# Optimization experiments

Measured on AMD Instinct MI355X. Metric: run time of the kernel, lower is better.

## Reference

```python
import jax, jax.numpy as jnp
import numpy as np

BIG_NEG = -1.0e6  # constants.big_negative


def setup_inputs() -> dict:
    key = jax.random.key(0)
    ks = jax.random.split(key, 10)
    B, N, NF, HNF, M, T = 2048, 100, 128, 128, 128, 12
    hidden_output_nodes = jax.random.normal(ks[0], (B, N, HNF), dtype=jnp.float32)
    input_nodes = jax.random.normal(ks[1], (B, N, NF), dtype=jnp.float32)
    node_mask = jax.random.uniform(ks[2], (B, N)) < 0.8
    node_mask = node_mask.at[:, 0].set(True)  # avoid fully-masked rows
    s = 0.05
    W_emb = jax.random.normal(ks[3], (M, NF + HNF), dtype=jnp.float32) * s
    b_emb = jnp.zeros((M,), dtype=jnp.float32)
    W_ih = jax.random.normal(ks[4], (4 * M, M), dtype=jnp.float32) * s
    b_ih = jnp.zeros((4 * M,), dtype=jnp.float32)
    W_hh = jax.random.normal(ks[5], (4 * M, M), dtype=jnp.float32) * s
    b_hh = jnp.zeros((4 * M,), dtype=jnp.float32)
    return {
        "hidden_output_nodes": hidden_output_nodes,
        "input_nodes": input_nodes,
        "W_emb": W_emb, "b_emb": b_emb,
        "W_ih": W_ih, "b_ih": b_ih, "W_hh": W_hh, "b_hh": b_hh,
        "node_mask": node_mask,
        "lstm_computations": T,
    }


def _set2vec(hidden_output_nodes, input_nodes, W_emb, b_emb, W_ih, b_ih, W_hh, b_hh, node_mask, T):
    B = input_nodes.shape[0]
    M = W_emb.shape[0]
    # memory: [B, N, M]
    cat = jnp.concatenate((hidden_output_nodes, input_nodes), axis=2)
    memory = jnp.einsum("bnf,mf->bnm", cat, W_emb) + b_emb
    energy_mask = (~node_mask).astype(memory.dtype) * BIG_NEG  # [B, N]

    zeros = jnp.zeros((B, M), dtype=memory.dtype)

    def step(carry, _):
        lstm_in, h, c = carry
        # LSTMCell (PyTorch gate order: i, f, g, o)
        gates = lstm_in @ W_ih.T + b_ih + h @ W_hh.T + b_hh
        i, f, g, o = jnp.split(gates, 4, axis=-1)
        c = jax.nn.sigmoid(f) * c + jax.nn.sigmoid(i) * jnp.tanh(g)
        q = jax.nn.sigmoid(o) * jnp.tanh(c)  # query / new hidden state
        # dot-product attention read over the node memory
        energies = jnp.einsum("bm,bnm->bn", q, memory) + energy_mask
        attn = jax.nn.softmax(energies, axis=1)
        read = jnp.einsum("bn,bnm->bm", attn, memory)
        return (read, q, c), None

    (read, q, _), _ = jax.lax.scan(step, (zeros, zeros, zeros), None, length=T)
    return jnp.concatenate((q, read), axis=1)  # [B, 2*M]


def reference(hidden_output_nodes, input_nodes, W_emb, b_emb, W_ih, b_ih, W_hh, b_hh, node_mask, lstm_computations):
    return _set2vec(hidden_output_nodes, input_nodes, W_emb, b_emb, W_ih, b_ih, W_hh, b_hh, node_mask, lstm_computations)
```

## Files before the change

### kernel.cpp

```cpp
#include <hip/hip_runtime.h>
#include <hip/hip_fp16.h>
#include <math.h>

#define BIG_NEG  (-1.0e6f)
#define NN   100
#define MD   128
#define KD   256
#define G4   512
#define NB   4
#define MP2  68
#define XPAD 288

#define WS_WGF_H  32768
#define WS_BIAS_F 81920

typedef _Float16 f16x2 __attribute__((ext_vector_type(2)));
typedef _Float16 f16x8 __attribute__((ext_vector_type(8)));
typedef float    f32x4 __attribute__((ext_vector_type(4)));

#if __has_builtin(__builtin_amdgcn_rcpf)
#define RCPF(x) __builtin_amdgcn_rcpf(x)
#else
#define RCPF(x) (1.0f / (x))
#endif

#define PKRTZ(a, b) __builtin_bit_cast(unsigned, __builtin_amdgcn_cvt_pkrtz((a), (b)))

__device__ __forceinline__ float sigm(float x) {
    return RCPF(1.0f + __expf(-x));
}
__device__ __forceinline__ float tanh_f(float x) {
    float xc = fminf(fmaxf(x, -15.0f), 15.0f);
    float e  = __expf(2.0f * xc);
    return (e - 1.0f) * RCPF(e + 1.0f);
}

extern "C" __global__ void prep_kernel(const float* __restrict__ W_emb,
                                       const float* __restrict__ W_ih,
                                       const float* __restrict__ b_ih,
                                       const float* __restrict__ W_hh,
                                       const float* __restrict__ b_hh,
                                       float* __restrict__ ws) {
    int tid = blockIdx.x * blockDim.x + threadIdx.x;
    int nth = gridDim.x * blockDim.x;
    __half* WF    = (__half*)ws;
    __half* WG    = (__half*)ws + WS_WGF_H;
    float*  biasc = ws + WS_BIAS_F;
    for (int i = tid; i < 32768; i += nth) {
        int kg = i >> 10, m = (i >> 3) & 127, j = i & 7;
        WF[i] = __float2half(W_emb[m * 256 + kg * 8 + j]);
    }
    for (int i = tid; i < 131072; i += nth) {
        int kc = i >> 12, g = (i >> 3) & 511, j = i & 7;
        int k = kc * 8 + j;
        float w = (k < 128) ? W_ih[g * 128 + k] : W_hh[g * 128 + (k - 128)];
        WG[i] = __float2half(w);
    }
    for (int i = tid; i < 512; i += nth) biasc[i] = b_ih[i] + b_hh[i];
}

extern "C" __global__ __launch_bounds__(1024, 4)
void set2vec_main(const float* __restrict__ hidden,
                  const float* __restrict__ input,
                  const float* __restrict__ b_emb,
                  const unsigned char* __restrict__ mask_bytes,
                  const int* __restrict__ Tptr,
                  const float* __restrict__ ws,
                  float* __restrict__ out) {
    __shared__ __half2 mem2[NB][NN][MP2];
    __shared__ __half  xcath[NB][XPAD];
    __shared__ float   xcat2[NB][KD];
    __shared__ float   cbuf[NB][MD];
    __shared__ float   emask[NB][NN];
    __shared__ float   bbuf[G4];
    __shared__ int     mask_is_u8;
    __shared__ float   gbuf[NB][G4];
    __shared__ float   ebuf[NB][128];
    __shared__ float   abuf[NB][NN];

    const int tid  = threadIdx.x;
    const int b0   = blockIdx.x * NB;
    const int lane = tid & 63, wv = tid >> 6;
    const int ln15 = lane & 15, lhi = lane >> 4;
    const __half* WF   = (const __half*)ws;
    const __half* memh = (const __half*)mem2;

    if (tid == 0) {
        int nz = 0;
        for (int i = 0; i < 64; ++i)
            if ((i & 3) && mask_bytes[i]) nz = 1;
        mask_is_u8 = nz;
    }

    {
        const float be0 = b_emb[0 * 16 + ln15], be1 = b_emb[1 * 16 + ln15];
        const float be2 = b_emb[2 * 16 + ln15], be3 = b_emb[3 * 16 + ln15];
        const float be4 = b_emb[4 * 16 + ln15], be5 = b_emb[5 * 16 + ln15];
        const float be6 = b_emb[6 * 16 + ln15], be7 = b_emb[7 * 16 + ln15];
        __half* memw = (__half*)mem2;
        for (int tile = wv; tile < 25; tile += 16) {
            f32x4 acc0 = {be0, be0, be0, be0}, acc1 = {be1, be1, be1, be1};
            f32x4 acc2 = {be2, be2, be2, be2}, acc3 = {be3, be3, be3, be3};
            f32x4 acc4 = {be4, be4, be4, be4}, acc5 = {be5, be5, be5, be5};
            f32x4 acc6 = {be6, be6, be6, be6}, acc7 = {be7, be7, be7, be7};

            const int rA     = tile * 16 + ln15;
            const int rAok   = rA < NB * NN;
            const long gbase = ((long)(b0 * NN + rA)) << 7;

            #pragma unroll 1
            for (int mk = 0; mk < 8; ++mk) {
                f16x8 aF;
                if (rAok) {
                    int k0 = mk * 32 + lhi * 8;
                    const float* src = (k0 < 128) ? (hidden + gbase + k0)
                                                  : (input + gbase + (k0 - 128));
                    float4 v0 = *(const float4*)src;
                    float4 v1 = *(const float4*)(src + 4);
                    union { f16x8 v; unsigned u[4]; } au;
                    au.u[0] = PKRTZ(v0.x, v0.y);
                    au.u[1] = PKRTZ(v0.z, v0.w);
                    au.u[2] = PKRTZ(v1.x, v1.y);
                    au.u[3] = PKRTZ(v1.z, v1.w);
                    aF = au.v;
                } else {
                    aF = (f16x8)(_Float16)0.0f;
                }
                const __half* wrow = WF + ((mk * 4 + lhi) * 128 + ln15) * 8;
#define EMB_CT(CT, ACC) { \
                union { uint4 u; f16x8 v; } bu; \
                bu.u = *(const uint4*)(wrow + (CT * 16) * 8); \
                ACC = __builtin_amdgcn_mfma_f32_16x16x32_f16(aF, bu.v, ACC, 0, 0, 0); }
                EMB_CT(0, acc0) EMB_CT(1, acc1) EMB_CT(2, acc2) EMB_CT(3, acc3)
                EMB_CT(4, acc4) EMB_CT(5, acc5) EMB_CT(6, acc6) EMB_CT(7, acc7)
#undef EMB_CT
            }
#define EMB_WR(CT, ACC) { \
            _Pragma("unroll") \
            for (int reg = 0; reg < 4; ++reg) { \
                int r = tile * 16 + lhi * 4 + reg; \
                if (r < NB * NN) { \
                    int bb = r / NN, n = r - (r / NN) * NN; \
                    memw[(bb * NN + n) * (2 * MP2) + CT * 16 + ln15] = __float2half(ACC[reg]); \
                } } }
            EMB_WR(0, acc0) EMB_WR(1, acc1) EMB_WR(2, acc2) EMB_WR(3, acc3)
            EMB_WR(4, acc4) EMB_WR(5, acc5) EMB_WR(6, acc6) EMB_WR(7, acc7)
#undef EMB_WR
        }
    }

    const uint4* WgB = (const uint4*)((const __half*)ws + WS_WGF_H);
    const int ct0 = wv * 2, ct1 = wv * 2 + 1;
#define LDW(KS) \
    const uint4 wA##KS = WgB[((KS) * 4 + lhi) * 512 + ct0 * 16 + ln15]; \
    const uint4 wB##KS = WgB[((KS) * 4 + lhi) * 512 + ct1 * 16 + ln15];
    LDW(0) LDW(1) LDW(2) LDW(3) LDW(4) LDW(5) LDW(6) LDW(7)
#undef LDW

    for (int i = tid; i < NB * XPAD; i += 1024) ((__half*)xcath)[i] = __float2half(0.0f);
    ((float*)xcat2)[tid] = 0.0f;
    if (tid < NB * MD) ((float*)cbuf)[tid] = 0.0f;
    if (tid < G4) bbuf[tid] = ws[WS_BIAS_F + tid];
    if (tid < NB * NN) {
        int bb = tid / NN, n = tid - bb * NN;
        long mrow = (long)(b0 + bb) * NN + n;
        int valid = mask_is_u8 ? (mask_bytes[mrow] != 0)
                               : (((const int*)mask_bytes)[mrow] != 0);
        emask[bb][n] = valid ? 0.0f : BIG_NEG;
    }
    __syncthreads();

    const int T = Tptr[0];

    const __half* aBase = &xcath[ln15 & 3][lhi * 8];

    const int ep0 = wv * 2, ep1 = wv * 2 + 1;
    const int e_bb0 = ep0 / 7, e_nt0 = ep0 - e_bb0 * 7;
    const int e_bb1 = ep1 / 7, e_nt1 = ep1 - e_bb1 * 7;
    const int e_n0  = e_nt0 * 16 + ln15, e_n1 = e_nt1 * 16 + ln15;
    const int e_n0c = (e_n0 < 100) ? e_n0 : 99;
    const int e_n1c = (e_n1 < 100) ? e_n1 : 99;
    const __half* eB0 = memh + (e_bb0 * NN + e_n0c) * (2 * MP2) + lhi * 8;
    const __half* eB1 = memh + (e_bb1 * NN + e_n1c) * (2 * MP2) + lhi * 8;
    const __half* eA0 = &xcath[e_bb0][128 + lhi * 8];
    const __half* eA1 = &xcath[e_bb1][128 + lhi * 8];

    const int sr_bb = (wv >> 1) & 3, sr_mh = wv & 1;
    const int rg = lane >> 3, rs = lane & 7;
    const int r_start = (rg <= 4) ? rg * 13 : 64 + (rg - 5) * 12;
    const int r_cnt   = (rg < 4) ? 13 : 12;
    const __half* rB = memh + sr_bb * NN * (2 * MP2) + sr_mh * 64 + rs * 8;

    for (int step = 0; step < T; ++step) {
        {
            f32x4 ga = {0.f, 0.f, 0.f, 0.f}, gb = {0.f, 0.f, 0.f, 0.f};
#define GS(KS) { \
            union { uint4 u; f16x8 v; } a, ba, bc; \
            a.u  = *(const uint4*)(aBase + (KS) * 32); \
            ba.u = wA##KS; bc.u = wB##KS; \
            ga = __builtin_amdgcn_mfma_f32_16x16x32_f16(a.v, ba.v, ga, 0, 0, 0); \
            gb = __builtin_amdgcn_mfma_f32_16x16x32_f16(a.v, bc.v, gb, 0, 0, 0); }
            GS(0) GS(1) GS(2) GS(3) GS(4) GS(5) GS(6) GS(7)
#undef GS
            if (lhi == 0) {
                #pragma unroll
                for (int r = 0; r < 4; ++r) {
                    gbuf[r][ct0 * 16 + ln15] = ga[r];
                    gbuf[r][ct1 * 16 + ln15] = gb[r];
                }
            }
        }
        __syncthreads();
        if (tid < NB * MD) {
            int bb = tid >> 7, m = tid & 127;
            float gi = gbuf[bb][m]       + bbuf[m];
            float gf = gbuf[bb][128 + m] + bbuf[128 + m];
            float gg = gbuf[bb][256 + m] + bbuf[256 + m];
            float go = gbuf[bb][384 + m] + bbuf[384 + m];
            float c  = cbuf[bb][m];
            c = sigm(gf) * c + sigm(gi) * tanh_f(gg);
            float qv = sigm(go) * tanh_f(c);
            cbuf[bb][m] = c;
            xcat2[bb][128 + m] = qv;
            xcath[bb][128 + m] = __float2half(qv);
        }
        __syncthreads();
        if (wv < 14) {
            f32x4 e0 = {0.f, 0.f, 0.f, 0.f}, e1 = {0.f, 0.f, 0.f, 0.f};
#define ES(KS) { \
            union { uint4 u; f16x8 v; } a0, a1, bq0, bq1; \
            a0.u  = *(const uint4*)(eA0 + (KS) * 32); \
            bq0.u = *(const uint4*)(eB0 + (KS) * 32); \
            a1.u  = *(const uint4*)(eA1 + (KS) * 32); \
            bq1.u = *(const uint4*)(eB1 + (KS) * 32); \
            e0 = __builtin_amdgcn_mfma_f32_16x16x32_f16(a0.v, bq0.v, e0, 0, 0, 0); \
            e1 = __builtin_amdgcn_mfma_f32_16x16x32_f16(a1.v, bq1.v, e1, 0, 0, 0); }
            ES(0) ES(1) ES(2) ES(3)
#undef ES
            if (lhi == 0) {
                if (e_n0 < 100) ebuf[e_bb0][e_n0] = e0[0] + emask[e_bb0][e_n0];
                if (e_n1 < 100) ebuf[e_bb1][e_n1] = e1[0] + emask[e_bb1][e_n1];
            }
        }
        __syncthreads();
        if (wv < 8) {
            {
                float e0 = ebuf[sr_bb][lane];
                float e1 = (lane < 36) ? ebuf[sr_bb][64 + lane] : -INFINITY;
                float mx = fmaxf(e0, e1);
                for (int off = 32; off; off >>= 1) mx = fmaxf(mx, __shfl_xor(mx, off, 64));
                float p0 = __expf(e0 - mx);
                float p1 = (lane < 36) ? __expf(e1 - mx) : 0.0f;
                float s = p0 + p1;
                for (int off = 32; off; off >>= 1) s += __shfl_xor(s, off, 64);
                float inv = RCPF(s);
                abuf[sr_bb][lane] = p0 * inv;
                if (lane < 36) abuf[sr_bb][64 + lane] = p1 * inv;
            }
            float a0 = 0.f, a1 = 0.f, a2 = 0.f, a3 = 0.f;
            float a4 = 0.f, a5 = 0.f, a6 = 0.f, a7 = 0.f;
            #pragma unroll
            for (int j = 0; j < 13; ++j) {
                if (j < r_cnt) {
                    int n = r_start + j;
                    float av = abuf[sr_bb][n];
                    uint4 u  = *(const uint4*)(rB + n * (2 * MP2));
                    float2 f0 = __half22float2(*(__half2*)&u.x);
                    float2 f1 = __half22float2(*(__half2*)&u.y);
                    float2 f2 = __half22float2(*(__half2*)&u.z);
                    float2 f3 = __half22float2(*(__half2*)&u.w);
                    a0 = fmaf(av, f0.x, a0); a1 = fmaf(av, f0.y, a1);
                    a2 = fmaf(av, f1.x, a2); a3 = fmaf(av, f1.y, a3);
                    a4 = fmaf(av, f2.x, a4); a5 = fmaf(av, f2.y, a5);
                    a6 = fmaf(av, f3.x, a6); a7 = fmaf(av, f3.y, a7);
                }
            }
#define RED(A) A += __shfl_xor(A, 8, 64); A += __shfl_xor(A, 16, 64); A += __shfl_xor(A, 32, 64);
            RED(a0) RED(a1) RED(a2) RED(a3) RED(a4) RED(a5) RED(a6) RED(a7)
#undef RED
            if (lane < 8) {
                int m = sr_mh * 64 + lane * 8;
                float4 lo = {a0, a1, a2, a3}, hi = {a4, a5, a6, a7};
                *(float4*)&xcat2[sr_bb][m]     = lo;
                *(float4*)&xcat2[sr_bb][m + 4] = hi;
                uint4 hv;
                hv.x = PKRTZ(a0, a1);
                hv.y = PKRTZ(a2, a3);
                hv.z = PKRTZ(a4, a5);
                hv.w = PKRTZ(a6, a7);
                *(uint4*)&xcath[sr_bb][m] = hv;
            }
        }
        __syncthreads();
    }

    {
        int bb = tid >> 8, j = tid & 255;
        float v = (j < 128) ? xcat2[bb][128 + j] : xcat2[bb][j - 128];
        out[((long)(b0 + bb) << 8) + j] = v;
    }
}

extern "C" void kernel_launch(void* const* d_in, const int* in_sizes, int n_in,
                              void* d_out, int out_size, void* d_ws, size_t ws_size,
                              hipStream_t stream) {
    const float* hidden = (const float*)d_in[0];
    const float* input  = (const float*)d_in[1];
    const float* W_emb  = (const float*)d_in[2];
    const float* b_emb  = (const float*)d_in[3];
    const float* W_ih   = (const float*)d_in[4];
    const float* b_ih   = (const float*)d_in[5];
    const float* W_hh   = (const float*)d_in[6];
    const float* b_hh   = (const float*)d_in[7];
    const unsigned char* mask = (const unsigned char*)d_in[8];
    const int*  Tptr    = (const int*)d_in[9];
    float* ws   = (float*)d_ws;
    float* outp = (float*)d_out;

    hipLaunchKernelGGL(prep_kernel, dim3(128), dim3(256), 0, stream,
                       W_emb, W_ih, b_ih, W_hh, b_hh, ws);
    hipLaunchKernelGGL(set2vec_main, dim3(512), dim3(1024), 0, stream,
                       hidden, input, b_emb, mask, Tptr, ws, outp);
}
```

Before: 165.5 us.

## Halve batch rows per block and reload LSTM weights each step

Cuts the batch elements per workgroup from 4 to 2 and doubles the grid to 1024 blocks. The embedding, energy and attention-read work is redistributed across waves to match. The per-wave register-resident gate weights are dropped, and weights are now reloaded from global memory (likely L2) at every LSTM step, freeing registers. The aim is more blocks in flight and lower per-block latency on the serial recurrence, at the cost of repeated weight traffic and MFMA tiles that are only half-used on rows.

```diff
diff --git a/kernel.cpp b/kernel.cpp
--- a/kernel.cpp
+++ b/kernel.cpp
@@ -7,7 +7,7 @@
 #define MD   128
 #define KD   256
 #define G4   512
-#define NB   4
+#define NB   2
 #define MP2  68
 #define XPAD 288
 
@@ -98,7 +98,8 @@
         const float be4 = b_emb[4 * 16 + ln15], be5 = b_emb[5 * 16 + ln15];
         const float be6 = b_emb[6 * 16 + ln15], be7 = b_emb[7 * 16 + ln15];
         __half* memw = (__half*)mem2;
-        for (int tile = wv; tile < 25; tile += 16) {
+        const int tile = wv;
+        if (tile < 13) {
             f32x4 acc0 = {be0, be0, be0, be0}, acc1 = {be1, be1, be1, be1};
             f32x4 acc2 = {be2, be2, be2, be2}, acc3 = {be3, be3, be3, be3};
             f32x4 acc4 = {be4, be4, be4, be4}, acc5 = {be5, be5, be5, be5};
@@ -151,14 +152,9 @@
 
     const uint4* WgB = (const uint4*)((const __half*)ws + WS_WGF_H);
     const int ct0 = wv * 2, ct1 = wv * 2 + 1;
-#define LDW(KS) \
-    const uint4 wA##KS = WgB[((KS) * 4 + lhi) * 512 + ct0 * 16 + ln15]; \
-    const uint4 wB##KS = WgB[((KS) * 4 + lhi) * 512 + ct1 * 16 + ln15];
-    LDW(0) LDW(1) LDW(2) LDW(3) LDW(4) LDW(5) LDW(6) LDW(7)
-#undef LDW
 
     for (int i = tid; i < NB * XPAD; i += 1024) ((__half*)xcath)[i] = __float2half(0.0f);
-    ((float*)xcat2)[tid] = 0.0f;
+    if (tid < NB * KD) ((float*)xcat2)[tid] = 0.0f;
     if (tid < NB * MD) ((float*)cbuf)[tid] = 0.0f;
     if (tid < G4) bbuf[tid] = ws[WS_BIAS_F + tid];
     if (tid < NB * NN) {
@@ -172,24 +168,20 @@
 
     const int T = Tptr[0];
 
-    const __half* aBase = &xcath[ln15 & 3][lhi * 8];
-
-    const int ep0 = wv * 2, ep1 = wv * 2 + 1;
-    const int e_bb0 = ep0 / 7, e_nt0 = ep0 - e_bb0 * 7;
-    const int e_bb1 = ep1 / 7, e_nt1 = ep1 - e_bb1 * 7;
-    const int e_n0  = e_nt0 * 16 + ln15, e_n1 = e_nt1 * 16 + ln15;
-    const int e_n0c = (e_n0 < 100) ? e_n0 : 99;
-    const int e_n1c = (e_n1 < 100) ? e_n1 : 99;
-    const __half* eB0 = memh + (e_bb0 * NN + e_n0c) * (2 * MP2) + lhi * 8;
-    const __half* eB1 = memh + (e_bb1 * NN + e_n1c) * (2 * MP2) + lhi * 8;
-    const __half* eA0 = &xcath[e_bb0][128 + lhi * 8];
-    const __half* eA1 = &xcath[e_bb1][128 + lhi * 8];
-
-    const int sr_bb = (wv >> 1) & 3, sr_mh = wv & 1;
-    const int rg = lane >> 3, rs = lane & 7;
-    const int r_start = (rg <= 4) ? rg * 13 : 64 + (rg - 5) * 12;
-    const int r_cnt   = (rg < 4) ? 13 : 12;
-    const __half* rB = memh + sr_bb * NN * (2 * MP2) + sr_mh * 64 + rs * 8;
+    const __half* aBase = &xcath[ln15 & 1][lhi * 8];
+
+    const int e_bb = (wv < 14) ? (wv / 7) : 0;
+    const int e_nt = (wv < 14) ? (wv - e_bb * 7) : 0;
+    const int e_n  = e_nt * 16 + ln15;
+    const int e_nc = (e_n < 100) ? e_n : 99;
+    const __half* eB = memh + (e_bb * NN + e_nc) * (2 * MP2) + lhi * 8;
+    const __half* eA = &xcath[e_bb][128 + lhi * 8];
+
+    const int sr_bb = (wv >> 2) & 1, sr_mq = wv & 3;
+    const int rg = lane >> 2, rs = lane & 3;
+    const int r_start = (rg < 4) ? rg * 7 : 28 + (rg - 4) * 6;
+    const int r_cnt   = (rg < 4) ? 7 : 6;
+    const __half* rB = memh + sr_bb * NN * (2 * MP2) + sr_mq * 32 + rs * 8;
 
     for (int step = 0; step < T; ++step) {
         {
@@ -197,17 +189,17 @@
 #define GS(KS) { \
             union { uint4 u; f16x8 v; } a, ba, bc; \
             a.u  = *(const uint4*)(aBase + (KS) * 32); \
-            ba.u = wA##KS; bc.u = wB##KS; \
+            ba.u = WgB[((KS) * 4 + lhi) * 512 + ct0 * 16 + ln15]; \
+            bc.u = WgB[((KS) * 4 + lhi) * 512 + ct1 * 16 + ln15]; \
             ga = __builtin_amdgcn_mfma_f32_16x16x32_f16(a.v, ba.v, ga, 0, 0, 0); \
             gb = __builtin_amdgcn_mfma_f32_16x16x32_f16(a.v, bc.v, gb, 0, 0, 0); }
             GS(0) GS(1) GS(2) GS(3) GS(4) GS(5) GS(6) GS(7)
 #undef GS
             if (lhi == 0) {
-                #pragma unroll
-                for (int r = 0; r < 4; ++r) {
-                    gbuf[r][ct0 * 16 + ln15] = ga[r];
-                    gbuf[r][ct1 * 16 + ln15] = gb[r];
-                }
+                gbuf[0][ct0 * 16 + ln15] = ga[0];
+                gbuf[1][ct0 * 16 + ln15] = ga[1];
+                gbuf[0][ct1 * 16 + ln15] = gb[0];
+                gbuf[1][ct1 * 16 + ln15] = gb[1];
             }
         }
         __syncthreads();
@@ -226,21 +218,16 @@
         }
         __syncthreads();
         if (wv < 14) {
-            f32x4 e0 = {0.f, 0.f, 0.f, 0.f}, e1 = {0.f, 0.f, 0.f, 0.f};
+            f32x4 e0 = {0.f, 0.f, 0.f, 0.f};
 #define ES(KS) { \
-            union { uint4 u; f16x8 v; } a0, a1, bq0, bq1; \
-            a0.u  = *(const uint4*)(eA0 + (KS) * 32); \
-            bq0.u = *(const uint4*)(eB0 + (KS) * 32); \
-            a1.u  = *(const uint4*)(eA1 + (KS) * 32); \
-            bq1.u = *(const uint4*)(eB1 + (KS) * 32); \
-            e0 = __builtin_amdgcn_mfma_f32_16x16x32_f16(a0.v, bq0.v, e0, 0, 0, 0); \
-            e1 = __builtin_amdgcn_mfma_f32_16x16x32_f16(a1.v, bq1.v, e1, 0, 0, 0); }
+            union { uint4 u; f16x8 v; } a0, bq0; \
+            a0.u  = *(const uint4*)(eA + (KS) * 32); \
+            bq0.u = *(const uint4*)(eB + (KS) * 32); \
+            e0 = __builtin_amdgcn_mfma_f32_16x16x32_f16(a0.v, bq0.v, e0, 0, 0, 0); }
             ES(0) ES(1) ES(2) ES(3)
 #undef ES
-            if (lhi == 0) {
-                if (e_n0 < 100) ebuf[e_bb0][e_n0] = e0[0] + emask[e_bb0][e_n0];
-                if (e_n1 < 100) ebuf[e_bb1][e_n1] = e1[0] + emask[e_bb1][e_n1];
-            }
+            if (lhi == 0 && e_n < 100)
+                ebuf[e_bb][e_n] = e0[0] + emask[e_bb][e_n];
         }
         __syncthreads();
         if (wv < 8) {
@@ -260,7 +247,7 @@
             float a0 = 0.f, a1 = 0.f, a2 = 0.f, a3 = 0.f;
             float a4 = 0.f, a5 = 0.f, a6 = 0.f, a7 = 0.f;
             #pragma unroll
-            for (int j = 0; j < 13; ++j) {
+            for (int j = 0; j < 7; ++j) {
                 if (j < r_cnt) {
                     int n = r_start + j;
                     float av = abuf[sr_bb][n];
@@ -275,11 +262,12 @@
                     a6 = fmaf(av, f3.x, a6); a7 = fmaf(av, f3.y, a7);
                 }
             }
-#define RED(A) A += __shfl_xor(A, 8, 64); A += __shfl_xor(A, 16, 64); A += __shfl_xor(A, 32, 64);
+#define RED(A) A += __shfl_xor(A, 4, 64); A += __shfl_xor(A, 8, 64); \
+               A += __shfl_xor(A, 16, 64); A += __shfl_xor(A, 32, 64);
             RED(a0) RED(a1) RED(a2) RED(a3) RED(a4) RED(a5) RED(a6) RED(a7)
 #undef RED
-            if (lane < 8) {
-                int m = sr_mh * 64 + lane * 8;
+            if (lane < 4) {
+                int m = sr_mq * 32 + lane * 8;
                 float4 lo = {a0, a1, a2, a3}, hi = {a4, a5, a6, a7};
                 *(float4*)&xcat2[sr_bb][m]     = lo;
                 *(float4*)&xcat2[sr_bb][m + 4] = hi;
@@ -294,7 +282,7 @@
         __syncthreads();
     }
 
-    {
+    if (tid < NB * 256) {
         int bb = tid >> 8, j = tid & 255;
         float v = (j < 128) ? xcat2[bb][128 + j] : xcat2[bb][j - 128];
         out[((long)(b0 + bb) << 8) + j] = v;
@@ -319,6 +307,6 @@
 
     hipLaunchKernelGGL(prep_kernel, dim3(128), dim3(256), 0, stream,
                        W_emb, W_ih, b_ih, W_hh, b_hh, ws);
-    hipLaunchKernelGGL(set2vec_main, dim3(512), dim3(1024), 0, stream,
+    hipLaunchKernelGGL(set2vec_main, dim3(1024), dim3(1024), 0, stream,
                        hidden, input, b_emb, mask, Tptr, ws, outp);
 }
```

Result: slower. 236.5 us (+42.9%).

## Fuse LSTM pointwise into gate MFMA via interleaved gates and double-buffered inputs

Applied to the files above, without the earlier changes.

Gate weight rows and biases are permuted so each 4-lane group holds the i,f,g,o gates for one hidden unit. The LSTM cell update then runs in registers via cross-lane shuffles right after the gate MFMA, which removes the gbuf round trip and one barrier per step. The LSTM input vector is double-buffered so the next step's q and read can be written without a race, and the attention read now spreads over all 16 waves with finer row splits. In exchange, the gate weights are reloaded from global memory every step instead of staying in registers, which adds memory latency in the recurrent loop.

```diff
diff --git a/kernel.cpp b/kernel.cpp
--- a/kernel.cpp
+++ b/kernel.cpp
@@ -51,12 +51,16 @@
         WF[i] = __float2half(W_emb[m * 256 + kg * 8 + j]);
     }
     for (int i = tid; i < 131072; i += nth) {
-        int kc = i >> 12, g = (i >> 3) & 511, j = i & 7;
+        int kc = i >> 12, gp = (i >> 3) & 511, j = i & 7;
         int k = kc * 8 + j;
+        int g = (gp & 3) * 128 + (gp >> 2);
         float w = (k < 128) ? W_ih[g * 128 + k] : W_hh[g * 128 + (k - 128)];
         WG[i] = __float2half(w);
     }
-    for (int i = tid; i < 512; i += nth) biasc[i] = b_ih[i] + b_hh[i];
+    for (int i = tid; i < 512; i += nth) {
+        int g = (i & 3) * 128 + (i >> 2);
+        biasc[i] = b_ih[g] + b_hh[g];
+    }
 }
 
 extern "C" __global__ __launch_bounds__(1024, 4)
@@ -68,13 +72,12 @@
                   const float* __restrict__ ws,
                   float* __restrict__ out) {
     __shared__ __half2 mem2[NB][NN][MP2];
-    __shared__ __half  xcath[NB][XPAD];
+    __shared__ __half  xh[2][NB][XPAD];
     __shared__ float   xcat2[NB][KD];
     __shared__ float   cbuf[NB][MD];
     __shared__ float   emask[NB][NN];
     __shared__ float   bbuf[G4];
     __shared__ int     mask_is_u8;
-    __shared__ float   gbuf[NB][G4];
     __shared__ float   ebuf[NB][128];
     __shared__ float   abuf[NB][NN];
 
@@ -151,13 +154,9 @@
 
     const uint4* WgB = (const uint4*)((const __half*)ws + WS_WGF_H);
     const int ct0 = wv * 2, ct1 = wv * 2 + 1;
-#define LDW(KS) \
-    const uint4 wA##KS = WgB[((KS) * 4 + lhi) * 512 + ct0 * 16 + ln15]; \
-    const uint4 wB##KS = WgB[((KS) * 4 + lhi) * 512 + ct1 * 16 + ln15];
-    LDW(0) LDW(1) LDW(2) LDW(3) LDW(4) LDW(5) LDW(6) LDW(7)
-#undef LDW
-
-    for (int i = tid; i < NB * XPAD; i += 1024) ((__half*)xcath)[i] = __float2half(0.0f);
+    const int gp0 = ct0 * 16 + ln15, gp1 = ct1 * 16 + ln15;
+
+    for (int i = tid; i < 2 * NB * XPAD; i += 1024) ((__half*)xh)[i] = __float2half(0.0f);
     ((float*)xcat2)[tid] = 0.0f;
     if (tid < NB * MD) ((float*)cbuf)[tid] = 0.0f;
     if (tid < G4) bbuf[tid] = ws[WS_BIAS_F + tid];
@@ -172,7 +171,12 @@
 
     const int T = Tptr[0];
 
-    const __half* aBase = &xcath[ln15 & 3][lhi * 8];
+    const __half* aB0 = &xh[0][ln15 & 3][lhi * 8];
+    const __half* aB1 = &xh[1][ln15 & 3][lhi * 8];
+
+    const int pw_wr = (ln15 & 3) == 0;
+    const int pw_m0 = ct0 * 4 + (ln15 >> 2);
+    const int pw_m1 = ct1 * 4 + (ln15 >> 2);
 
     const int ep0 = wv * 2, ep1 = wv * 2 + 1;
     const int e_bb0 = ep0 / 7, e_nt0 = ep0 - e_bb0 * 7;
@@ -182,50 +186,69 @@
     const int e_n1c = (e_n1 < 100) ? e_n1 : 99;
     const __half* eB0 = memh + (e_bb0 * NN + e_n0c) * (2 * MP2) + lhi * 8;
     const __half* eB1 = memh + (e_bb1 * NN + e_n1c) * (2 * MP2) + lhi * 8;
-    const __half* eA0 = &xcath[e_bb0][128 + lhi * 8];
-    const __half* eA1 = &xcath[e_bb1][128 + lhi * 8];
-
-    const int sr_bb = (wv >> 1) & 3, sr_mh = wv & 1;
-    const int rg = lane >> 3, rs = lane & 7;
-    const int r_start = (rg <= 4) ? rg * 13 : 64 + (rg - 5) * 12;
-    const int r_cnt   = (rg < 4) ? 13 : 12;
-    const __half* rB = memh + sr_bb * NN * (2 * MP2) + sr_mh * 64 + rs * 8;
+    const __half* eA00 = &xh[0][e_bb0][128 + lhi * 8];
+    const __half* eA01 = &xh[1][e_bb0][128 + lhi * 8];
+    const __half* eA10 = &xh[0][e_bb1][128 + lhi * 8];
+    const __half* eA11 = &xh[1][e_bb1][128 + lhi * 8];
+
+    const int sr_bb = wv >> 2, sr_mq = wv & 3;
+    const int rg = lane >> 2, rs = lane & 3;
+    const int r_start = (rg < 4) ? rg * 7 : 28 + (rg - 4) * 6;
+    const int r_cnt   = (rg < 4) ? 7 : 6;
+    const __half* rB = memh + sr_bb * NN * (2 * MP2) + sr_mq * 32 + rs * 8;
+
+#define SHFL4(D, S, MSK) { D[0] = __shfl_xor(S[0], MSK, 64); D[1] = __shfl_xor(S[1], MSK, 64); \
+                           D[2] = __shfl_xor(S[2], MSK, 64); D[3] = __shfl_xor(S[3], MSK, 64); }
+#define SEL4(V) (lhi == 0 ? V[0] : (lhi == 1 ? V[1] : (lhi == 2 ? V[2] : V[3])))
 
     for (int step = 0; step < T; ++step) {
+        const int sp = step & 1;
+        const __half* aB = sp ? aB1 : aB0;
+        __half (*xhN)[XPAD] = xh[sp ^ 1];
+
         {
             f32x4 ga = {0.f, 0.f, 0.f, 0.f}, gb = {0.f, 0.f, 0.f, 0.f};
 #define GS(KS) { \
             union { uint4 u; f16x8 v; } a, ba, bc; \
-            a.u  = *(const uint4*)(aBase + (KS) * 32); \
-            ba.u = wA##KS; bc.u = wB##KS; \
+            a.u  = *(const uint4*)(aB + (KS) * 32); \
+            ba.u = WgB[((KS) * 4 + lhi) * 512 + gp0]; \
+            bc.u = WgB[((KS) * 4 + lhi) * 512 + gp1]; \
             ga = __builtin_amdgcn_mfma_f32_16x16x32_f16(a.v, ba.v, ga, 0, 0, 0); \
             gb = __builtin_amdgcn_mfma_f32_16x16x32_f16(a.v, bc.v, gb, 0, 0, 0); }
             GS(0) GS(1) GS(2) GS(3) GS(4) GS(5) GS(6) GS(7)
 #undef GS
-            if (lhi == 0) {
-                #pragma unroll
-                for (int r = 0; r < 4; ++r) {
-                    gbuf[r][ct0 * 16 + ln15] = ga[r];
-                    gbuf[r][ct1 * 16 + ln15] = gb[r];
-                }
-            }
-        }
-        __syncthreads();
-        if (tid < NB * MD) {
-            int bb = tid >> 7, m = tid & 127;
-            float gi = gbuf[bb][m]       + bbuf[m];
-            float gf = gbuf[bb][128 + m] + bbuf[128 + m];
-            float gg = gbuf[bb][256 + m] + bbuf[256 + m];
-            float go = gbuf[bb][384 + m] + bbuf[384 + m];
-            float c  = cbuf[bb][m];
-            c = sigm(gf) * c + sigm(gi) * tanh_f(gg);
-            float qv = sigm(go) * tanh_f(c);
-            cbuf[bb][m] = c;
-            xcat2[bb][128 + m] = qv;
-            xcath[bb][128 + m] = __float2half(qv);
+            {
+                float b0v = bbuf[gp0], b1v = bbuf[gp1];
+                ga[0] += b0v; ga[1] += b0v; ga[2] += b0v; ga[3] += b0v;
+                gb[0] += b1v; gb[1] += b1v; gb[2] += b1v; gb[3] += b1v;
+            }
+            f32x4 aV1, aV2, aV3, bV1, bV2, bV3;
+            SHFL4(aV1, ga, 1) SHFL4(aV2, ga, 2) SHFL4(aV3, aV1, 2)
+            SHFL4(bV1, gb, 1) SHFL4(bV2, gb, 2) SHFL4(bV3, bV1, 2)
+            if (pw_wr) {
+                float gi = SEL4(ga),  gf = SEL4(aV1), gg = SEL4(aV2), go = SEL4(aV3);
+                float c  = cbuf[lhi][pw_m0];
+                c = sigm(gf) * c + sigm(gi) * tanh_f(gg);
+                float qv = sigm(go) * tanh_f(c);
+                cbuf[lhi][pw_m0] = c;
+                xhN[lhi][128 + pw_m0] = __float2half(qv);
+                xcat2[lhi][128 + pw_m0] = qv;
+
+                float hi_ = SEL4(gb), hf = SEL4(bV1), hg = SEL4(bV2), ho = SEL4(bV3);
+                float c1  = cbuf[lhi][pw_m1];
+                c1 = sigm(hf) * c1 + sigm(hi_) * tanh_f(hg);
+                float qv1 = sigm(ho) * tanh_f(c1);
+                cbuf[lhi][pw_m1] = c1;
+                xhN[lhi][128 + pw_m1] = __float2half(qv1);
+                xcat2[lhi][128 + pw_m1] = qv1;
+            }
         }
         __syncthreads();
         if (wv < 14) {
+            const __half* eA0 = sp ? eA01 : eA00;
+            const __half* eA1 = sp ? eA11 : eA10;
+            eA0 = (sp ^ 1) ? eA01 : eA00;
+            eA1 = (sp ^ 1) ? eA11 : eA10;
             f32x4 e0 = {0.f, 0.f, 0.f, 0.f}, e1 = {0.f, 0.f, 0.f, 0.f};
 #define ES(KS) { \
             union { uint4 u; f16x8 v; } a0, a1, bq0, bq1; \
@@ -243,7 +266,7 @@
             }
         }
         __syncthreads();
-        if (wv < 8) {
+        {
             {
                 float e0 = ebuf[sr_bb][lane];
                 float e1 = (lane < 36) ? ebuf[sr_bb][64 + lane] : -INFINITY;
@@ -260,7 +283,7 @@
             float a0 = 0.f, a1 = 0.f, a2 = 0.f, a3 = 0.f;
             float a4 = 0.f, a5 = 0.f, a6 = 0.f, a7 = 0.f;
             #pragma unroll
-            for (int j = 0; j < 13; ++j) {
+            for (int j = 0; j < 7; ++j) {
                 if (j < r_cnt) {
                     int n = r_start + j;
                     float av = abuf[sr_bb][n];
@@ -275,11 +298,12 @@
                     a6 = fmaf(av, f3.x, a6); a7 = fmaf(av, f3.y, a7);
                 }
             }
-#define RED(A) A += __shfl_xor(A, 8, 64); A += __shfl_xor(A, 16, 64); A += __shfl_xor(A, 32, 64);
+#define RED(A) A += __shfl_xor(A, 4, 64); A += __shfl_xor(A, 8, 64); \
+               A += __shfl_xor(A, 16, 64); A += __shfl_xor(A, 32, 64);
             RED(a0) RED(a1) RED(a2) RED(a3) RED(a4) RED(a5) RED(a6) RED(a7)
 #undef RED
-            if (lane < 8) {
-                int m = sr_mh * 64 + lane * 8;
+            if (lane < 4) {
+                int m = sr_mq * 32 + lane * 8;
                 float4 lo = {a0, a1, a2, a3}, hi = {a4, a5, a6, a7};
                 *(float4*)&xcat2[sr_bb][m]     = lo;
                 *(float4*)&xcat2[sr_bb][m + 4] = hi;
@@ -288,7 +312,7 @@
                 hv.y = PKRTZ(a2, a3);
                 hv.z = PKRTZ(a4, a5);
                 hv.w = PKRTZ(a6, a7);
-                *(uint4*)&xcath[sr_bb][m] = hv;
+                *(uint4*)&xhN[sr_bb][m] = hv;
             }
         }
         __syncthreads();
```

New measurement: 206.8 us. +24.9%, slower.
